# Optimization experiments

Hardware: AMD Instinct MI355X
Metric: run time of the kernel (lower is better)

The kernel has to match this reference:

```python
import jax, jax.numpy as jnp
import numpy as np

LAMBDA_D = 250.0
POS_MARGIN = 1.0
NEG_MARGIN = 0.2
BLOCK = 8          # block_size in the original
DIST_THRESH = 7.5  # correspondence threshold in pixels
EPS = 1e-12        # F.normalize eps


def _l2_normalize(x, axis):
    # matches torch.nn.functional.normalize: x / max(||x||_2, eps)
    n = jnp.linalg.norm(x, axis=axis, keepdims=True)
    return x / jnp.maximum(n, EPS)


def setup_inputs() -> dict:
    key = jax.random.key(0)
    k1, k2, k3 = jax.random.split(key, 3)
    b, d, hc, wc = 2, 256, 60, 80  # 480x640 image, block 8
    desc = jax.random.normal(k1, (b, d, hc, wc), dtype=jnp.float32)
    wrap_desc = jax.random.normal(k2, (b, d, hc, wc), dtype=jnp.float32)
    # realistic near-identity homographies (random H would warp everything off-image)
    H = jnp.eye(3, dtype=jnp.float32)[None] + 0.02 * jax.random.normal(k3, (b, 3, 3), dtype=jnp.float32)
    return {"desc": desc, "wrap_desc": wrap_desc, "H": H}


def reference(desc, wrap_desc, H):
    b, d, hc, wc = desc.shape
    n = hc * wc

    # cell-center coordinates in (row, col) order, shape (hc, wc, 2)
    coords = jnp.stack(
        jnp.meshgrid(jnp.arange(hc), jnp.arange(wc), indexing="ij"), axis=-1
    ).astype(jnp.float32) * BLOCK + BLOCK // 2

    # homogeneous (x, y, 1) points, shape (n, 3)
    xy1 = jnp.concatenate(
        [coords[..., 1:2], coords[..., 0:1], jnp.ones((hc, wc, 1), jnp.float32)],
        axis=-1,
    ).reshape(n, 3)

    # warp by homography: (b, n, 3)
    w = jnp.einsum("bij,nj->bni", H, xy1)
    wxy = w[..., :2] / w[..., 2:3]                       # (b, n, 2) in (x, y)
    warp = jnp.stack([wxy[..., 1], wxy[..., 0]], axis=-1).reshape(b, hc, wc, 2)  # (row, col)

    # distance between warped query centers and all cell centers: (b, hc, wc, hc, wc)
    dist = jnp.linalg.norm(coords[None, None, None] - warp[:, :, :, None, None, :], axis=-1)
    S = (dist <= DIST_THRESH).astype(desc.dtype)

    # unit-normalized descriptors, channel-last
    dn = _l2_normalize(jnp.transpose(desc, (0, 2, 3, 1)), axis=-1)       # (b, hc, wc, d)
    wn = _l2_normalize(jnp.transpose(wrap_desc, (0, 2, 3, 1)), axis=-1)  # (b, hc, wc, d)

    # full correlation volume via batched GEMM (same math as broadcast-sum)
    dot = jax.nn.relu(jnp.einsum("bijd,bkld->bijkl", dn, wn))           # (b,hc,wc,hc,wc)

    # normalize over warped-cell axis (k, l), then over query-cell axis (i, j)
    dot = _l2_normalize(dot.reshape(b, hc, wc, n), axis=3).reshape(b, hc, wc, hc, wc)
    dot = _l2_normalize(dot.reshape(b, n, hc, wc), axis=1).reshape(b, hc, wc, hc, wc)

    loss = LAMBDA_D * S * jax.nn.relu(POS_MARGIN - dot) + (1.0 - S) * jax.nn.relu(dot - NEG_MARGIN)
    # sum over (i,j,k,l) per image / n^2, then sum over batch == total sum / n^2
    return jnp.sum(loss) / float(n * n)
```

## Files before the change

### kernel.cpp

```cpp
#include <hip/hip_runtime.h>

#define HC 60
#define WCC 80
#define NCELL 4800
#define NP 4864
#define NB 38
#define DCH 256
#define BATCH 2
#define QT 64

typedef _Float16 half8 __attribute__((ext_vector_type(8)));
typedef _Float16 half2v __attribute__((ext_vector_type(2)));
typedef float f32x4 __attribute__((ext_vector_type(4)));

__device__ __forceinline__ void gload_lds16(const void* gp, void* lp) {
  __builtin_amdgcn_global_load_lds(
      (const __attribute__((address_space(1))) void*)gp,
      (__attribute__((address_space(3))) void*)lp, 16, 0, 0);
}

__global__ __launch_bounds__(256) void warp_kernel(const float* __restrict__ H,
                                                   float* __restrict__ wout) {
  int idx = blockIdx.x * 256 + threadIdx.x;
  if (idx >= BATCH * NP) return;
  int b = idx / NP;
  int q = idx - b * NP;
  float wr = 1e9f, wc = 1e9f;
  if (q < NCELL) {
    int i = q / WCC;
    int j = q - i * WCC;
    float x = (float)(j * 8 + 4);
    float y = (float)(i * 8 + 4);
    const float* h = H + b * 9;
    float w0 = h[0] * x + h[1] * y + h[2];
    float w1 = h[3] * x + h[4] * y + h[5];
    float w2 = h[6] * x + h[7] * y + h[8];
    wr = w1 / w2;
    wc = w0 / w2;
  }
  wout[2 * idx]     = wr;
  wout[2 * idx + 1] = wc;
}

__global__ __launch_bounds__(256) void normalize_kernel(
    const float* __restrict__ desc, const float* __restrict__ wdesc,
    _Float16* __restrict__ dnp, _Float16* __restrict__ wnp) {
  __shared__ _Float16 vt[DCH][QT + 2];
  __shared__ float pss[4][QT];
  __shared__ float invq[QT];
  const int q0 = blockIdx.x * QT;
  const int which = blockIdx.y;
  const int b = blockIdx.z;
  const float* in = which ? wdesc : desc;
  _Float16* out = which ? wnp : dnp;
  const int tx = threadIdx.x & 63;
  const int ty = threadIdx.x >> 6;
  const int q = q0 + tx;
  float ss = 0.f;
  for (int cc = 0; cc < DCH / 4; ++cc) {
    const int c = cc * 4 + ty;
    float v = (q < NCELL) ? in[((size_t)b * DCH + c) * NCELL + q] : 0.f;
    vt[c][tx] = (_Float16)v;
    ss += v * v;
  }
  pss[ty][tx] = ss;
  __syncthreads();
  if (ty == 0) {
    float tot = pss[0][tx] + pss[1][tx] + pss[2][tx] + pss[3][tx];
    invq[tx] = 1.f / fmaxf(sqrtf(tot), 1e-12f);
  }
  __syncthreads();
  for (int it = 0; it < QT; ++it) {
    out[((size_t)b * NP + q0 + it) * DCH + threadIdx.x] =
        (_Float16)((float)vt[threadIdx.x][it] * invq[it]);
  }
}

template <int MODE, bool STOREU>
__global__ __launch_bounds__(256) void gemm_kernel(
    const _Float16* __restrict__ A, const _Float16* __restrict__ Bm,
    const float* __restrict__ invr, const float* __restrict__ colscale,
    const float* __restrict__ warp, float* __restrict__ sqacc,
    float* __restrict__ lossp, _Float16* __restrict__ uout) {
  __shared__ _Float16 As[2][128][64];
  __shared__ _Float16 Bs[2][128][64];
  const int tid = threadIdx.x;
  const int wave = tid >> 6;
  const int lane = tid & 63;
  const int batch = blockIdx.z;
  const int row0 = blockIdx.y * 128;
  const int col0 = blockIdx.x * 128;
  const _Float16* Ab = A + ((size_t)batch * NP + row0) * DCH;
  const _Float16* Bb = Bm + ((size_t)batch * NP + col0) * DCH;

  const int wq_r = wave >> 1;
  const int wq_c = wave & 1;
  const int g = lane >> 4;
  const int cL = lane & 15;

  f32x4 acc[4][4] = {};

  const int srow = lane >> 3;
  const int scol = lane & 7;
  const int sc_swz = (scol ^ srow) * 8;

  auto stage = [&](int ks, int buf) {
#pragma unroll
    for (int c = 0; c < 4; ++c) {
      const int chunk = wave * 4 + c;
      const int r = chunk * 8 + srow;
      gload_lds16(Ab + (size_t)r * DCH + ks * 64 + sc_swz,
                  (char*)(&As[buf][0][0]) + chunk * 1024);
      gload_lds16(Bb + (size_t)r * DCH + ks * 64 + sc_swz,
                  (char*)(&Bs[buf][0][0]) + chunk * 1024);
    }
  };

  stage(0, 0);
  __syncthreads();

#pragma unroll
  for (int ks = 0; ks < 4; ++ks) {
    if (ks < 3) stage(ks + 1, (ks + 1) & 1);
    const int buf = ks & 1;
#pragma unroll
    for (int kk = 0; kk < 2; ++kk) {
      half8 af[4], bf[4];
#pragma unroll
      for (int m = 0; m < 4; ++m) {
        const int row = wq_r * 64 + m * 16 + cL;
        const int c16 = (kk * 4 + g) ^ (row & 7);
        af[m] = *reinterpret_cast<const half8*>(
            (const char*)(&As[buf][0][0]) + row * 128 + c16 * 16);
      }
#pragma unroll
      for (int n = 0; n < 4; ++n) {
        const int row = wq_c * 64 + n * 16 + cL;
        const int c16 = (kk * 4 + g) ^ (row & 7);
        bf[n] = *reinterpret_cast<const half8*>(
            (const char*)(&Bs[buf][0][0]) + row * 128 + c16 * 16);
      }
#pragma unroll
      for (int m = 0; m < 4; ++m)
#pragma unroll
        for (int n = 0; n < 4; ++n)
          acc[m][n] =
              __builtin_amdgcn_mfma_f32_16x16x32_f16(af[m], bf[n], acc[m][n], 0, 0, 0);
    }
    __syncthreads();
  }

  if (MODE == 0 || MODE == 1) {
    float cs[4];
    if (MODE == 1) {
#pragma unroll
      for (int n = 0; n < 4; ++n)
        cs[n] = colscale[(size_t)batch * NP + col0 + wq_c * 64 + n * 16 + cL];
    }
    float rs[4][4];
#pragma unroll
    for (int m = 0; m < 4; ++m)
#pragma unroll
      for (int j = 0; j < 4; ++j) rs[m][j] = 0.f;
#pragma unroll
    for (int m = 0; m < 4; ++m)
#pragma unroll
      for (int n = 0; n < 4; ++n)
#pragma unroll
        for (int j = 0; j < 4; ++j) {
          float u = fmaxf(acc[m][n][j], 0.f);
          if (MODE == 1) u *= cs[n];
          rs[m][j] += u * u;
        }
#pragma unroll
    for (int m = 0; m < 4; ++m)
#pragma unroll
      for (int j = 0; j < 4; ++j) {
        float v = rs[m][j];
        v += __shfl_xor(v, 1, 64);
        v += __shfl_xor(v, 2, 64);
        v += __shfl_xor(v, 4, 64);
        v += __shfl_xor(v, 8, 64);
        if (cL == 0)
          atomicAdd(&sqacc[(size_t)batch * NP + row0 + wq_r * 64 + m * 16 + g * 4 + j], v);
      }
    if (STOREU) {
#pragma unroll
      for (int m = 0; m < 4; ++m)
#pragma unroll
        for (int j = 0; j < 4; ++j) {
          const size_t r = (size_t)batch * NP + row0 + wq_r * 64 + m * 16 + g * 4 + j;
#pragma unroll
          for (int n = 0; n < 4; ++n) {
            const int c = col0 + wq_c * 64 + n * 16 + cL;
            uout[r * NP + c] = (_Float16)fmaxf(acc[m][n][j], 0.f);
          }
        }
    }
  } else if (MODE == 2) {
    float cy[4], cx[4], ic[4];
    int cvalid[4];
#pragma unroll
    for (int n = 0; n < 4; ++n) {
      int ct = col0 + wq_c * 64 + n * 16 + cL;
      cvalid[n] = (ct < NCELL);
      int tk = ct / WCC;
      int tl = ct - tk * WCC;
      cy[n] = (float)(tk * 8 + 4);
      cx[n] = (float)(tl * 8 + 4);
      ic[n] = colscale[(size_t)batch * NP + ct];
    }
    float lsum = 0.f;
#pragma unroll
    for (int m = 0; m < 4; ++m)
#pragma unroll
      for (int j = 0; j < 4; ++j) {
        const int rq = row0 + wq_r * 64 + m * 16 + g * 4 + j;
        if (rq < NCELL) {
          const float ir = invr[(size_t)batch * NP + rq];
          const float wr = warp[((size_t)batch * NP + rq) * 2];
          const float wcol = warp[((size_t)batch * NP + rq) * 2 + 1];
#pragma unroll
          for (int n = 0; n < 4; ++n) {
            if (cvalid[n]) {
              float u = fmaxf(acc[m][n][j], 0.f);
              float v = u * ir * ic[n];
              float dr = cy[n] - wr;
              float dc = cx[n] - wcol;
              float pos = 250.f * fmaxf(1.f - v, 0.f);
              float neg = fmaxf(v - 0.2f, 0.f);
              lsum += (dr * dr + dc * dc <= 56.25f) ? pos : neg;
            }
          }
        }
      }
#pragma unroll
    for (int s = 1; s < 64; s <<= 1) lsum += __shfl_xor(lsum, s, 64);
    if (lane == 0) {
      int slot = (((batch * NB + blockIdx.y) * NB + blockIdx.x) << 2) | wave;
      lossp[slot] = lsum;
    }
  }
}

__global__ __launch_bounds__(256) void passB_kernel(const _Float16* __restrict__ u,
                                                    const float* __restrict__ r2,
                                                    float* __restrict__ c2) {
  const int b = blockIdx.z;
  const int t0 = blockIdx.x * 512 + threadIdx.x * 2;
  if (t0 >= NP) return;
  const int q0 = blockIdx.y * (NP / 64);
  const _Float16* up = u + ((size_t)b * NP + q0) * NP + t0;
  const float* r2p = r2 + b * NP + q0;
  float s0 = 0.f, s1 = 0.f;
  for (int q = 0; q < NP / 64; ++q) {
    float ir = 1.f / fmaxf(sqrtf(r2p[q]), 1e-12f);
    half2v h = *reinterpret_cast<const half2v*>(up);
    float v0 = (float)h[0] * ir;
    float v1 = (float)h[1] * ir;
    s0 += v0 * v0;
    s1 += v1 * v1;
    up += NP;
  }
  atomicAdd(&c2[b * NP + t0], s0);
  atomicAdd(&c2[b * NP + t0 + 1], s1);
}

__global__ __launch_bounds__(256) void passC_kernel(const _Float16* __restrict__ u,
                                                    const float* __restrict__ r2,
                                                    const float* __restrict__ c2,
                                                    const float* __restrict__ warp,
                                                    float* __restrict__ lossp) {
  const int b = blockIdx.z;
  const int t0 = blockIdx.x * 512 + threadIdx.x * 2;
  const int q0 = blockIdx.y * (NP / 32);
  float cy[2], cx[2], ic[2];
  bool val[2];
#pragma unroll
  for (int i = 0; i < 2; ++i) {
    const int t = t0 + i;
    const bool v = (t0 < NP) && (t < NCELL);
    val[i] = v;
    const int tk = t / WCC;
    const int tl = t - tk * WCC;
    cy[i] = (float)(tk * 8 + 4);
    cx[i] = (float)(tl * 8 + 4);
    ic[i] = v ? 1.f / fmaxf(sqrtf(c2[b * NP + t]), 1e-12f) : 0.f;
  }
  float lsum = 0.f;
  if (t0 < NP) {
    const _Float16* up = u + ((size_t)b * NP + q0) * NP + t0;
    for (int q = 0; q < NP / 32; ++q) {
      const int qq = q0 + q;
      const float ir = 1.f / fmaxf(sqrtf(r2[b * NP + qq]), 1e-12f);
      const float wr = warp[(size_t)(b * NP + qq) * 2];
      const float wc = warp[(size_t)(b * NP + qq) * 2 + 1];
      half2v h = *reinterpret_cast<const half2v*>(up);
#pragma unroll
      for (int i = 0; i < 2; ++i) {
        if (val[i]) {
          float v = (float)h[i] * ir * ic[i];
          float dr = cy[i] - wr;
          float dc = cx[i] - wc;
          float pos = 250.f * fmaxf(1.f - v, 0.f);
          float neg = fmaxf(v - 0.2f, 0.f);
          lsum += (dr * dr + dc * dc <= 56.25f) ? pos : neg;
        }
      }
      up += NP;
    }
  }
#pragma unroll
  for (int s = 1; s < 64; s <<= 1) lsum += __shfl_xor(lsum, s, 64);
  if ((threadIdx.x & 63) == 0) {
    int slot = ((((b * 32 + blockIdx.y) * 10 + blockIdx.x) << 2) | (threadIdx.x >> 6));
    lossp[slot] = lsum;
  }
}

__global__ void finalize_inv(const float* __restrict__ sq, float* __restrict__ inv,
                             int count) {
  int i = blockIdx.x * 256 + threadIdx.x;
  if (i < count) inv[i] = 1.f / fmaxf(sqrtf(sq[i]), 1e-12f);
}

__global__ __launch_bounds__(1024) void loss_reduce(const float* __restrict__ lossp,
                                                    float* __restrict__ out, int count) {
  double s = 0.0;
  for (int i = threadIdx.x; i < count; i += 1024) s += (double)lossp[i];
#pragma unroll
  for (int k = 1; k < 64; k <<= 1) s += __shfl_xor(s, k, 64);
  __shared__ double sd[16];
  if ((threadIdx.x & 63) == 0) sd[threadIdx.x >> 6] = s;
  __syncthreads();
  if (threadIdx.x == 0) {
    double t = 0.0;
    for (int w = 0; w < 16; ++w) t += sd[w];
    out[0] = (float)(t / ((double)NCELL * (double)NCELL));
  }
}

extern "C" void kernel_launch(void* const* d_in, const int* in_sizes, int n_in,
                              void* d_out, int out_size, void* d_ws, size_t ws_size,
                              hipStream_t stream) {
  const float* desc  = (const float*)d_in[0];
  const float* wdesc = (const float*)d_in[1];
  const float* H     = (const float*)d_in[2];
  char* ws = (char*)d_ws;

  constexpr size_t SZ_HALF = (size_t)BATCH * NP * DCH * sizeof(_Float16);
  constexpr size_t SZ_WARP = (size_t)BATCH * NP * 2 * sizeof(float);
  constexpr size_t SZ_VEC  = (size_t)BATCH * NP * sizeof(float);
  constexpr size_t SZ_LOSS = (size_t)BATCH * NB * NB * 4 * sizeof(float);
  constexpr size_t SZ_U    = (size_t)BATCH * NP * NP * sizeof(_Float16);
  constexpr size_t OFF_DNP  = 0;
  constexpr size_t OFF_WNP  = OFF_DNP + SZ_HALF;
  constexpr size_t OFF_WARP = OFF_WNP + SZ_HALF;
  constexpr size_t OFF_R2   = OFF_WARP + SZ_WARP;
  constexpr size_t OFF_INVR = OFF_R2 + SZ_VEC;
  constexpr size_t OFF_C2   = OFF_INVR + SZ_VEC;
  constexpr size_t OFF_INVC = OFF_C2 + SZ_VEC;
  constexpr size_t OFF_LOSS = OFF_INVC + SZ_VEC;
  constexpr size_t OFF_U    = OFF_LOSS + SZ_LOSS;
  constexpr size_t TOTAL    = OFF_U + SZ_U;

  _Float16* dnp = (_Float16*)(ws + OFF_DNP);
  _Float16* wnp = (_Float16*)(ws + OFF_WNP);
  float* warp = (float*)(ws + OFF_WARP);
  float* r2   = (float*)(ws + OFF_R2);
  float* invr = (float*)(ws + OFF_INVR);
  float* c2   = (float*)(ws + OFF_C2);
  float* invc = (float*)(ws + OFF_INVC);
  float* lossp = (float*)(ws + OFF_LOSS);
  _Float16* u = (_Float16*)(ws + OFF_U);

  hipMemsetAsync(r2, 0, 4 * SZ_VEC, stream);

  warp_kernel<<<dim3((BATCH * NP + 255) / 256), 256, 0, stream>>>(H, warp);
  normalize_kernel<<<dim3(NP / QT, 2, BATCH), 256, 0, stream>>>(desc, wdesc, dnp, wnp);

  dim3 gg(NB, NB, BATCH);
  if (ws_size >= TOTAL) {
    gemm_kernel<0, true><<<gg, 256, 0, stream>>>(dnp, wnp, nullptr, nullptr, nullptr,
                                                 r2, nullptr, u);
    passB_kernel<<<dim3(10, 64, BATCH), 256, 0, stream>>>(u, r2, c2);
    passC_kernel<<<dim3(10, 32, BATCH), 256, 0, stream>>>(u, r2, c2, warp, lossp);
    loss_reduce<<<1, 1024, 0, stream>>>(lossp, (float*)d_out, BATCH * 32 * 10 * 4);
  } else {
    gemm_kernel<0, false><<<gg, 256, 0, stream>>>(dnp, wnp, nullptr, nullptr, nullptr,
                                                  r2, nullptr, nullptr);
    finalize_inv<<<(BATCH * NP + 255) / 256, 256, 0, stream>>>(r2, invr, BATCH * NP);
    gemm_kernel<1, false><<<gg, 256, 0, stream>>>(wnp, dnp, nullptr, invr, nullptr,
                                                  c2, nullptr, nullptr);
    finalize_inv<<<(BATCH * NP + 255) / 256, 256, 0, stream>>>(c2, invc, BATCH * NP);
    gemm_kernel<2, false><<<gg, 256, 0, stream>>>(dnp, wnp, invr, invc, warp,
                                                  nullptr, lossp, nullptr);
    loss_reduce<<<1, 1024, 0, stream>>>(lossp, (float*)d_out, BATCH * NB * NB * 4);
  }
}
```

Before: 268.3 us.

## Stage relu'd GEMM output through LDS and vectorize passB/passC loads

The GEMM epilogue now writes the relu'd fp16 tile into shared memory, which reuses the operand buffers through a union, and then stores it with coalesced 16-byte rows instead of scattered 2-byte stores. To make the union fit, the K-loop drops double buffering and syncs after each stage. passB and passC read 8 halves per thread with half8 loads and use inverse norms precomputed by extra finalize_inv launches, so they no longer redo sqrt and divide per element. The cost is lost load/compute overlap in the GEMM, two extra small kernel launches, and a changed grid shape.

New measurement: 298.5 us. 11.2% more time.

```diff
diff --git a/kernel.cpp b/kernel.cpp
--- a/kernel.cpp
+++ b/kernel.cpp
@@ -10,7 +10,6 @@
 #define QT 64
 
 typedef _Float16 half8 __attribute__((ext_vector_type(8)));
-typedef _Float16 half2v __attribute__((ext_vector_type(2)));
 typedef float f32x4 __attribute__((ext_vector_type(4)));
 
 __device__ __forceinline__ void gload_lds16(const void* gp, void* lp) {
@@ -76,14 +75,18 @@
   }
 }
 
+union GemmSmem {
+  struct { _Float16 As[128][64]; _Float16 Bs[128][64]; } g;
+  _Float16 rp[128][132];
+};
+
 template <int MODE, bool STOREU>
 __global__ __launch_bounds__(256) void gemm_kernel(
     const _Float16* __restrict__ A, const _Float16* __restrict__ Bm,
     const float* __restrict__ invr, const float* __restrict__ colscale,
     const float* __restrict__ warp, float* __restrict__ sqacc,
     float* __restrict__ lossp, _Float16* __restrict__ uout) {
-  __shared__ _Float16 As[2][128][64];
-  __shared__ _Float16 Bs[2][128][64];
+  __shared__ GemmSmem sm;
   const int tid = threadIdx.x;
   const int wave = tid >> 6;
   const int lane = tid & 63;
@@ -104,25 +107,17 @@
   const int scol = lane & 7;
   const int sc_swz = (scol ^ srow) * 8;
 
-  auto stage = [&](int ks, int buf) {
+  for (int ks = 0; ks < 4; ++ks) {
 #pragma unroll
     for (int c = 0; c < 4; ++c) {
       const int chunk = wave * 4 + c;
       const int r = chunk * 8 + srow;
       gload_lds16(Ab + (size_t)r * DCH + ks * 64 + sc_swz,
-                  (char*)(&As[buf][0][0]) + chunk * 1024);
+                  (char*)(&sm.g.As[0][0]) + chunk * 1024);
       gload_lds16(Bb + (size_t)r * DCH + ks * 64 + sc_swz,
-                  (char*)(&Bs[buf][0][0]) + chunk * 1024);
-    }
-  };
-
-  stage(0, 0);
-  __syncthreads();
-
-#pragma unroll
-  for (int ks = 0; ks < 4; ++ks) {
-    if (ks < 3) stage(ks + 1, (ks + 1) & 1);
-    const int buf = ks & 1;
+                  (char*)(&sm.g.Bs[0][0]) + chunk * 1024);
+    }
+    __syncthreads();
 #pragma unroll
     for (int kk = 0; kk < 2; ++kk) {
       half8 af[4], bf[4];
@@ -131,14 +126,14 @@
         const int row = wq_r * 64 + m * 16 + cL;
         const int c16 = (kk * 4 + g) ^ (row & 7);
         af[m] = *reinterpret_cast<const half8*>(
-            (const char*)(&As[buf][0][0]) + row * 128 + c16 * 16);
+            (const char*)(&sm.g.As[0][0]) + row * 128 + c16 * 16);
       }
 #pragma unroll
       for (int n = 0; n < 4; ++n) {
         const int row = wq_c * 64 + n * 16 + cL;
         const int c16 = (kk * 4 + g) ^ (row & 7);
         bf[n] = *reinterpret_cast<const half8*>(
-            (const char*)(&Bs[buf][0][0]) + row * 128 + c16 * 16);
+            (const char*)(&sm.g.Bs[0][0]) + row * 128 + c16 * 16);
       }
 #pragma unroll
       for (int m = 0; m < 4; ++m)
@@ -188,14 +183,21 @@
 #pragma unroll
       for (int m = 0; m < 4; ++m)
 #pragma unroll
-        for (int j = 0; j < 4; ++j) {
-          const size_t r = (size_t)batch * NP + row0 + wq_r * 64 + m * 16 + g * 4 + j;
-#pragma unroll
-          for (int n = 0; n < 4; ++n) {
-            const int c = col0 + wq_c * 64 + n * 16 + cL;
-            uout[r * NP + c] = (_Float16)fmaxf(acc[m][n][j], 0.f);
-          }
-        }
+        for (int n = 0; n < 4; ++n)
+#pragma unroll
+          for (int j = 0; j < 4; ++j)
+            sm.rp[wq_r * 64 + m * 16 + g * 4 + j][wq_c * 64 + n * 16 + cL] =
+                (_Float16)fmaxf(acc[m][n][j], 0.f);
+      __syncthreads();
+      const int rl = tid >> 4;
+      const int uu = tid & 15;
+#pragma unroll
+      for (int p = 0; p < 8; ++p) {
+        const int row = p * 16 + rl;
+        half8 hv = *reinterpret_cast<const half8*>(&sm.rp[row][uu * 8]);
+        *reinterpret_cast<half8*>(
+            &uout[((size_t)batch * NP + row0 + row) * NP + col0 + uu * 8]) = hv;
+      }
     }
   } else if (MODE == 2) {
     float cy[4], cx[4], ic[4];
@@ -244,60 +246,63 @@
 }
 
 __global__ __launch_bounds__(256) void passB_kernel(const _Float16* __restrict__ u,
-                                                    const float* __restrict__ r2,
+                                                    const float* __restrict__ invr,
                                                     float* __restrict__ c2) {
   const int b = blockIdx.z;
-  const int t0 = blockIdx.x * 512 + threadIdx.x * 2;
+  const int t0 = blockIdx.x * 2048 + threadIdx.x * 8;
   if (t0 >= NP) return;
-  const int q0 = blockIdx.y * (NP / 64);
+  const int q0 = blockIdx.y * 64;
   const _Float16* up = u + ((size_t)b * NP + q0) * NP + t0;
-  const float* r2p = r2 + b * NP + q0;
-  float s0 = 0.f, s1 = 0.f;
-  for (int q = 0; q < NP / 64; ++q) {
-    float ir = 1.f / fmaxf(sqrtf(r2p[q]), 1e-12f);
-    half2v h = *reinterpret_cast<const half2v*>(up);
-    float v0 = (float)h[0] * ir;
-    float v1 = (float)h[1] * ir;
-    s0 += v0 * v0;
-    s1 += v1 * v1;
+  const float* irp = invr + b * NP + q0;
+  float s[8];
+#pragma unroll
+  for (int i = 0; i < 8; ++i) s[i] = 0.f;
+  for (int q = 0; q < 64; ++q) {
+    const float ir = irp[q];
+    half8 h = *reinterpret_cast<const half8*>(up);
+#pragma unroll
+    for (int i = 0; i < 8; ++i) {
+      float v = (float)h[i] * ir;
+      s[i] += v * v;
+    }
     up += NP;
   }
-  atomicAdd(&c2[b * NP + t0], s0);
-  atomicAdd(&c2[b * NP + t0 + 1], s1);
+#pragma unroll
+  for (int i = 0; i < 8; ++i) atomicAdd(&c2[b * NP + t0 + i], s[i]);
 }
 
 __global__ __launch_bounds__(256) void passC_kernel(const _Float16* __restrict__ u,
-                                                    const float* __restrict__ r2,
-                                                    const float* __restrict__ c2,
+                                                    const float* __restrict__ invr,
+                                                    const float* __restrict__ invc,
                                                     const float* __restrict__ warp,
                                                     float* __restrict__ lossp) {
   const int b = blockIdx.z;
-  const int t0 = blockIdx.x * 512 + threadIdx.x * 2;
-  const int q0 = blockIdx.y * (NP / 32);
-  float cy[2], cx[2], ic[2];
-  bool val[2];
-#pragma unroll
-  for (int i = 0; i < 2; ++i) {
-    const int t = t0 + i;
-    const bool v = (t0 < NP) && (t < NCELL);
-    val[i] = v;
+  const int t0 = blockIdx.x * 2048 + threadIdx.x * 8;
+  const int q0 = blockIdx.y * 128;
+  float cy[8], cx[8], ic[8];
+  bool val[8];
+  const bool active = (t0 < NP);
+#pragma unroll
+  for (int i = 0; i < 8; ++i) {
+    const int t = active ? (t0 + i) : 0;
+    val[i] = active && (t < NCELL);
     const int tk = t / WCC;
     const int tl = t - tk * WCC;
     cy[i] = (float)(tk * 8 + 4);
     cx[i] = (float)(tl * 8 + 4);
-    ic[i] = v ? 1.f / fmaxf(sqrtf(c2[b * NP + t]), 1e-12f) : 0.f;
+    ic[i] = invc[b * NP + t];
   }
   float lsum = 0.f;
-  if (t0 < NP) {
+  if (active) {
     const _Float16* up = u + ((size_t)b * NP + q0) * NP + t0;
-    for (int q = 0; q < NP / 32; ++q) {
+    for (int q = 0; q < 128; ++q) {
       const int qq = q0 + q;
-      const float ir = 1.f / fmaxf(sqrtf(r2[b * NP + qq]), 1e-12f);
+      const float ir = invr[b * NP + qq];
       const float wr = warp[(size_t)(b * NP + qq) * 2];
       const float wc = warp[(size_t)(b * NP + qq) * 2 + 1];
-      half2v h = *reinterpret_cast<const half2v*>(up);
-#pragma unroll
-      for (int i = 0; i < 2; ++i) {
+      half8 h = *reinterpret_cast<const half8*>(up);
+#pragma unroll
+      for (int i = 0; i < 8; ++i) {
         if (val[i]) {
           float v = (float)h[i] * ir * ic[i];
           float dr = cy[i] - wr;
@@ -313,7 +318,7 @@
 #pragma unroll
   for (int s = 1; s < 64; s <<= 1) lsum += __shfl_xor(lsum, s, 64);
   if ((threadIdx.x & 63) == 0) {
-    int slot = ((((b * 32 + blockIdx.y) * 10 + blockIdx.x) << 2) | (threadIdx.x >> 6));
+    int slot = ((((b * 38 + blockIdx.y) * 3 + blockIdx.x) << 2) | (threadIdx.x >> 6));
     lossp[slot] = lsum;
   }
 }
@@ -383,9 +388,11 @@
   if (ws_size >= TOTAL) {
     gemm_kernel<0, true><<<gg, 256, 0, stream>>>(dnp, wnp, nullptr, nullptr, nullptr,
                                                  r2, nullptr, u);
-    passB_kernel<<<dim3(10, 64, BATCH), 256, 0, stream>>>(u, r2, c2);
-    passC_kernel<<<dim3(10, 32, BATCH), 256, 0, stream>>>(u, r2, c2, warp, lossp);
-    loss_reduce<<<1, 1024, 0, stream>>>(lossp, (float*)d_out, BATCH * 32 * 10 * 4);
+    finalize_inv<<<(BATCH * NP + 255) / 256, 256, 0, stream>>>(r2, invr, BATCH * NP);
+    passB_kernel<<<dim3(3, 76, BATCH), 256, 0, stream>>>(u, invr, c2);
+    finalize_inv<<<(BATCH * NP + 255) / 256, 256, 0, stream>>>(c2, invc, BATCH * NP);
+    passC_kernel<<<dim3(3, 38, BATCH), 256, 0, stream>>>(u, invr, invc, warp, lossp);
+    loss_reduce<<<1, 1024, 0, stream>>>(lossp, (float*)d_out, BATCH * 38 * 3 * 4);
   } else {
     gemm_kernel<0, false><<<gg, 256, 0, stream>>>(dnp, wnp, nullptr, nullptr, nullptr,
                                                   r2, nullptr, nullptr);
```
